# Kernel tuning notes

Measured on AMD Instinct MI355X. Metric: run time of the kernel, lower is better.

Reference implementation:

```python
import jax, jax.numpy as jnp
import numpy as np

B, T, DIN, H, HB = 256, 512, 64, 256, 128  # batch, seq, input, hidden, bi-hidden


def rnn_layer(x, wih, whh, bih, bhh):
    # PyTorch nn.RNN (tanh) layer, batch_first. x: [B,T,I] -> [B,T,H]
    xw = jnp.einsum('bti,hi->bth', x, wih) + bih
    h0 = jnp.zeros((x.shape[0], whh.shape[0]), x.dtype)
    def step(h, xt):
        h = jnp.tanh(xt + h @ whh.T + bhh)
        return h, h
    _, ys = jax.lax.scan(step, h0, jnp.swapaxes(xw, 0, 1))
    return jnp.swapaxes(ys, 0, 1)


def gru_layer(x, wih, whh, bih, bhh, reverse=False):
    # PyTorch nn.GRU layer (gate order r,z,n). x: [B,T,I] -> [B,T,Hh]
    Hh = whh.shape[1]
    xg = jnp.einsum('bti,gi->btg', x, wih) + bih  # [B,T,3Hh]
    h0 = jnp.zeros((x.shape[0], Hh), x.dtype)
    def step(h, xt):
        hg = h @ whh.T + bhh
        xr, xz, xn = jnp.split(xt, 3, axis=-1)
        hr, hz, hn = jnp.split(hg, 3, axis=-1)
        r = jax.nn.sigmoid(xr + hr)
        z = jax.nn.sigmoid(xz + hz)
        n = jnp.tanh(xn + r * hn)
        h = (1.0 - z) * n + z * h
        return h, h
    _, ys = jax.lax.scan(step, h0, jnp.swapaxes(xg, 0, 1), reverse=reverse)
    return jnp.swapaxes(ys, 0, 1)


def setup_inputs() -> dict:
    key = jax.random.key(0)
    ks = iter(jax.random.split(key, 40))
    s = 0.05
    def w(shape):
        return jax.random.normal(next(ks), shape, jnp.float32) * s
    inp = {"x": jax.random.normal(next(ks), (B, T, DIN), jnp.float32)}
    inp.update(dict(
        rnn_wih0=w((H, DIN)), rnn_whh0=w((H, H)), rnn_bih0=w((H,)), rnn_bhh0=w((H,)),
        rnn_wih1=w((H, H)), rnn_whh1=w((H, H)), rnn_bih1=w((H,)), rnn_bhh1=w((H,)),
        gru_wih=w((2, 3 * H, H)), gru_whh=w((2, 3 * H, H)),
        gru_bih=w((2, 3 * H)), gru_bhh=w((2, 3 * H)),
        # bi-GRU: index order [l0_fwd, l0_bwd, l1_fwd, l1_bwd]; all inputs have width H
        bi_wih=w((4, 3 * HB, H)), bi_whh=w((4, 3 * HB, HB)),
        bi_bih=w((4, 3 * HB)), bi_bhh=w((4, 3 * HB)),
        att_w1=w((H // 2, H)), att_b1=w((H // 2,)), att_w2=w((1, H // 2)), att_b2=w((1,)),
        bn_gamma=jnp.ones((H,), jnp.float32), bn_beta=jnp.zeros((H,), jnp.float32),
        bn_mean=jnp.zeros((H,), jnp.float32), bn_var=jnp.ones((H,), jnp.float32),
        fc_w1=w((H // 2, H)), fc_b1=w((H // 2,)),
        fc_w2=w((H // 4, H // 2)), fc_b2=w((H // 4,)),
        fc_w3=w((1, H // 4)), fc_b3=w((1,)),
    ))
    return inp


def reference(x, rnn_wih0, rnn_whh0, rnn_bih0, rnn_bhh0,
              rnn_wih1, rnn_whh1, rnn_bih1, rnn_bhh1,
              gru_wih, gru_whh, gru_bih, gru_bhh,
              bi_wih, bi_whh, bi_bih, bi_bhh,
              att_w1, att_b1, att_w2, att_b2,
              bn_gamma, bn_beta, bn_mean, bn_var,
              fc_w1, fc_b1, fc_w2, fc_b2, fc_w3, fc_b3):
    # --- stacked tanh RNN (2 layers); dropout is identity in eval ---
    h = rnn_layer(x, rnn_wih0, rnn_whh0, rnn_bih0, rnn_bhh0)
    h = rnn_layer(h, rnn_wih1, rnn_whh1, rnn_bih1, rnn_bhh1)
    # --- stacked GRU (2 layers) ---
    for l in range(2):
        h = gru_layer(h, gru_wih[l], gru_whh[l], gru_bih[l], gru_bhh[l])
    # --- bidirectional GRU (2 layers, hidden HB per direction) ---
    for l in range(2):
        f = gru_layer(h, bi_wih[2 * l], bi_whh[2 * l], bi_bih[2 * l], bi_bhh[2 * l])
        b = gru_layer(h, bi_wih[2 * l + 1], bi_whh[2 * l + 1], bi_bih[2 * l + 1], bi_bhh[2 * l + 1], reverse=True)
        h = jnp.concatenate([f, b], axis=-1)  # [B,T,H]
    # --- additive attention pooling over time ---
    scores = jnp.tanh(h @ att_w1.T + att_b1) @ att_w2.T + att_b2  # [B,T,1]
    weights = jax.nn.softmax(scores, axis=1)
    ctx = jnp.sum(weights * h, axis=1)  # [B,H]
    # --- batchnorm (eval mode: running stats) ---
    ctx = (ctx - bn_mean) / jnp.sqrt(bn_var + 1e-5) * bn_gamma + bn_beta
    # --- FC head ---
    o = jax.nn.relu(ctx @ fc_w1.T + fc_b1)
    o = jax.nn.relu(o @ fc_w2.T + fc_b2)
    return o @ fc_w3.T + fc_b3  # [B,1]
```

## Files before the change

### kernel.cpp

```cpp
#include <hip/hip_runtime.h>


typedef short sv8 __attribute__((ext_vector_type(8)));
typedef short sv4 __attribute__((ext_vector_type(4)));
typedef float fv4 __attribute__((ext_vector_type(4)));

__device__ __forceinline__ float bf2f(short s) {
  union { unsigned u; float f; } v; v.u = ((unsigned)(unsigned short)s) << 16; return v.f;
}
__device__ __forceinline__ short f2bf(float f) {
  union { float f; unsigned u; } v; v.f = f;
  unsigned r = (v.u + 0x7fffu + ((v.u >> 16) & 1u)) >> 16;
  return (short)r;
}
__device__ __forceinline__ float sigm(float x) { return 1.f / (1.f + __expf(-x)); }
__device__ __forceinline__ float tanh_f(float x) {
  float ax = fabsf(x);
  float e = __expf(2.f * ax);
  float t = 1.f - 2.f / (e + 1.f);
  return copysignf(t, x);
}

__global__ __launch_bounds__(256) void f2b4(const float* __restrict__ s,
                                            short* __restrict__ d, int n4) {
  int i = blockIdx.x * 256 + threadIdx.x;
  if (i < n4) {
    fv4 v = ((const fv4*)s)[i];
    sv4 o;
    o[0] = f2bf(v[0]); o[1] = f2bf(v[1]); o[2] = f2bf(v[2]); o[3] = f2bf(v[3]);
    ((sv4*)d)[i] = o;
  }
}

__global__ __launch_bounds__(256) void bias_prep(
    const float* __restrict__ rbih0, const float* __restrict__ rbhh0,
    const float* __restrict__ rbih1, const float* __restrict__ rbhh1,
    const float* __restrict__ gbih, const float* __restrict__ gbhh,
    const float* __restrict__ bbih, const float* __restrict__ bbhh,
    float* __restrict__ BC) {
  int i = blockIdx.x * 256 + threadIdx.x;
  if (i >= 3584) return;
  float v;
  if (i < 256)       v = rbih0[i] + rbhh0[i];
  else if (i < 512)  { int c = i - 256; v = rbih1[c] + rbhh1[c]; }
  else if (i < 2048) { int j = i - 512; int c = j % 768;
                       v = gbih[j] + (c < 512 ? gbhh[j] : 0.f); }
  else               { int j = i - 2048; int c = j % 384;
                       v = bbih[j] + (c < 256 ? bbhh[j] : 0.f); }
  BC[i] = v;
}

template <int KS, int ACT, bool AF32>
__global__ __launch_bounds__(256, 4) void gemm_xw(
    const void* __restrict__ Av, const short* __restrict__ W,
    const float* __restrict__ bias, short* __restrict__ C,
    int N, int ldc, int w0, int l2tc) {
  const int K = KS * 32;
  const int lane = threadIdx.x & 63, wv = threadIdx.x >> 6;
  const int l15 = lane & 15, q = lane >> 4;
  const int m0 = blockIdx.x * 128 + wv * 32;
  const int tcm = (1 << l2tc) - 1;

  sv8 af[2][KS];
#pragma unroll
  for (int s = 0; s < 2; ++s) {
    const int r = m0 + s * 16 + l15;
    const size_t arow = (size_t)(r >> l2tc) * 512 + w0 + (r & tcm);
    if (AF32) {
      const float* ap = (const float*)Av + arow * K + q * 8;
#pragma unroll
      for (int k = 0; k < KS; ++k) {
        fv4 lo = *(const fv4*)(ap + k * 32);
        fv4 hi = *(const fv4*)(ap + k * 32 + 4);
        sv8 o;
        o[0] = f2bf(lo[0]); o[1] = f2bf(lo[1]); o[2] = f2bf(lo[2]); o[3] = f2bf(lo[3]);
        o[4] = f2bf(hi[0]); o[5] = f2bf(hi[1]); o[6] = f2bf(hi[2]); o[7] = f2bf(hi[3]);
        af[s][k] = o;
      }
    } else {
      const short* ap = (const short*)Av + arow * K + q * 8;
#pragma unroll
      for (int k = 0; k < KS; ++k) af[s][k] = *(const sv8*)(ap + k * 32);
    }
  }
  const int N16 = N >> 4;
  for (int nt = 0; nt < N16; ++nt) {
    const short* wp = W + (size_t)(nt * 16 + l15) * K + q * 8;
    fv4 acc0 = {0.f, 0.f, 0.f, 0.f}, acc1 = {0.f, 0.f, 0.f, 0.f};
#pragma unroll
    for (int k = 0; k < KS; ++k) {
      sv8 bf = *(const sv8*)(wp + k * 32);
      acc0 = __builtin_amdgcn_mfma_f32_16x16x32_bf16(af[0][k], bf, acc0, 0, 0, 0);
      acc1 = __builtin_amdgcn_mfma_f32_16x16x32_bf16(af[1][k], bf, acc1, 0, 0, 0);
    }
    float bv = bias[nt * 16 + l15];
#pragma unroll
    for (int s = 0; s < 2; ++s) {
      fv4 a = s ? acc1 : acc0;
#pragma unroll
      for (int j = 0; j < 4; ++j) {
        float v = a[j] + bv;
        if (ACT == 1) v = tanh_f(v);
        int row = m0 + s * 16 + q * 4 + j;
        C[(size_t)row * ldc + nt * 16 + l15] = f2bf(v);
      }
    }
  }
}

__global__ __launch_bounds__(256, 1) void rnn_scan(
    const short* __restrict__ xg, const short* __restrict__ whh,
    short* __restrict__ hout, int w0, int Tc, int first,
    short* __restrict__ hst) {
  constexpr int T = 512, H = 256, NR = 8, SP = H + 8;
  __shared__ __align__(16) short hl[NR * H];
  __shared__ __align__(16) float S[NR * SP];
  const int tid = threadIdx.x, lane = tid & 63, wv = tid >> 6;
  const int l15 = lane & 15, q = lane >> 4;
  const int r0 = blockIdx.x * NR;

  sv8 wf[4][8];
#pragma unroll
  for (int s = 0; s < 4; ++s) {
    const short* wp = whh + (size_t)(wv * 64 + s * 16 + l15) * H + q * 8;
#pragma unroll
    for (int k = 0; k < 8; ++k) wf[s][k] = *(const sv8*)(wp + k * 32);
  }
  const int brow = tid >> 5, bcb = tid & 31;
  const int hlo = brow * H + ((bcb * 8) ^ (brow << 3));
  const size_t xbase = ((size_t)(r0 + brow) * Tc) * H + bcb * 8;
  const size_t obase = ((size_t)(r0 + brow) * T + w0) * H + bcb * 8;

  sv8 hvv;
  if (first) { sv8 z = {0,0,0,0,0,0,0,0}; hvv = z; }
  else hvv = *(const sv8*)(hst + (size_t)(r0 + brow) * H + bcb * 8);
  *(sv8*)&hl[hlo] = hvv;
  sv8 xr = *(const sv8*)(xg + xbase);
  __syncthreads();

  const int arow = l15 & 7;
  const short* hb = hl + arow * H;
  const int asw = arow << 3;

  for (int t = 0; t < Tc; ++t) {
    fv4 acc[4] = {{0,0,0,0},{0,0,0,0},{0,0,0,0},{0,0,0,0}};
#pragma unroll
    for (int k = 0; k < 8; ++k) {
      sv8 a = *(const sv8*)(hb + ((k * 32 + q * 8) ^ asw));
#pragma unroll
      for (int s = 0; s < 4; ++s)
        acc[s] = __builtin_amdgcn_mfma_f32_16x16x32_bf16(a, wf[s][k], acc[s], 0, 0, 0);
    }
    if (q < 2) {
#pragma unroll
      for (int s = 0; s < 4; ++s)
#pragma unroll
        for (int j = 0; j < 4; ++j)
          S[(q * 4 + j) * SP + wv * 64 + s * 16 + l15] = acc[s][j];
    }
    __syncthreads();
    const float* sp = &S[brow * SP + bcb * 8];
    fv4 slo = *(const fv4*)sp, shi = *(const fv4*)(sp + 4);
    sv8 o;
#pragma unroll
    for (int i = 0; i < 4; ++i) o[i] = f2bf(tanh_f(bf2f(xr[i]) + slo[i]));
#pragma unroll
    for (int i = 0; i < 4; ++i) o[4 + i] = f2bf(tanh_f(bf2f(xr[4 + i]) + shi[i]));
    hvv = o;
    *(sv8*)&hl[hlo] = o;
    *(sv8*)(hout + obase + (size_t)t * H) = o;
    if (t + 1 < Tc) xr = *(const sv8*)(xg + xbase + (size_t)(t + 1) * H);
    __syncthreads();
  }
  *(sv8*)(hst + (size_t)(r0 + brow) * H + bcb * 8) = hvv;
}

__global__ __launch_bounds__(256, 1) void gru_scan(
    const short* __restrict__ xg, const short* __restrict__ whh,
    const float* __restrict__ bhn, short* __restrict__ hout,
    int w0, int Tc, int first, short* __restrict__ hst) {
  constexpr int T = 512, H = 256, G = 768, NR = 8, SP = H + 8;
  __shared__ __align__(16) short hl[NR * H];
  __shared__ __align__(16) float S[3 * NR * SP];
  const int tid = threadIdx.x, lane = tid & 63, wv = tid >> 6;
  const int l15 = lane & 15, q = lane >> 4;
  const int r0 = blockIdx.x * NR;

  sv8 wf[3][4][8];
#pragma unroll
  for (int g = 0; g < 3; ++g)
#pragma unroll
    for (int s = 0; s < 4; ++s) {
      const short* wp = whh + (size_t)(g * H + wv * 64 + s * 16 + l15) * H + q * 8;
#pragma unroll
      for (int k = 0; k < 8; ++k) wf[g][s][k] = *(const sv8*)(wp + k * 32);
    }
  const int brow = tid >> 5, bcb = tid & 31;
  const int hlo = brow * H + ((bcb * 8) ^ (brow << 3));
  const size_t xbase = ((size_t)(r0 + brow) * Tc) * G + bcb * 8;
  const size_t obase = ((size_t)(r0 + brow) * T + w0) * H + bcb * 8;
  const float* bp = bhn + bcb * 8;
  fv4 bn0 = *(const fv4*)bp, bn1 = *(const fv4*)(bp + 4);

  sv8 hp;
  if (first) { sv8 z = {0,0,0,0,0,0,0,0}; hp = z; }
  else hp = *(const sv8*)(hst + (size_t)(r0 + brow) * H + bcb * 8);
  *(sv8*)&hl[hlo] = hp;
  sv8 xr0 = *(const sv8*)(xg + xbase);
  sv8 xr1 = *(const sv8*)(xg + xbase + 256);
  sv8 xr2 = *(const sv8*)(xg + xbase + 512);
  __syncthreads();

  const int arow = l15 & 7;
  const short* hb = hl + arow * H;
  const int asw = arow << 3;

  for (int t = 0; t < Tc; ++t) {
    fv4 acc[3][4];
#pragma unroll
    for (int g = 0; g < 3; ++g)
#pragma unroll
      for (int s = 0; s < 4; ++s) acc[g][s] = (fv4){0,0,0,0};
#pragma unroll
    for (int k = 0; k < 8; ++k) {
      sv8 a = *(const sv8*)(hb + ((k * 32 + q * 8) ^ asw));
#pragma unroll
      for (int g = 0; g < 3; ++g)
#pragma unroll
        for (int s = 0; s < 4; ++s)
          acc[g][s] = __builtin_amdgcn_mfma_f32_16x16x32_bf16(a, wf[g][s][k], acc[g][s], 0, 0, 0);
    }
    if (q < 2) {
#pragma unroll
      for (int g = 0; g < 3; ++g)
#pragma unroll
        for (int s = 0; s < 4; ++s)
#pragma unroll
          for (int j = 0; j < 4; ++j)
            S[(g * NR + q * 4 + j) * SP + wv * 64 + s * 16 + l15] = acc[g][s][j];
    }
    __syncthreads();
    const float* s0 = &S[(0 * NR + brow) * SP + bcb * 8];
    const float* s1 = &S[(1 * NR + brow) * SP + bcb * 8];
    const float* s2 = &S[(2 * NR + brow) * SP + bcb * 8];
    fv4 r0v = *(const fv4*)s0, r1v = *(const fv4*)(s0 + 4);
    fv4 z0v = *(const fv4*)s1, z1v = *(const fv4*)(s1 + 4);
    fv4 n0v = *(const fv4*)s2, n1v = *(const fv4*)(s2 + 4);
    sv8 o;
#pragma unroll
    for (int i = 0; i < 4; ++i) {
      float rr = sigm(bf2f(xr0[i]) + r0v[i]);
      float zz = sigm(bf2f(xr1[i]) + z0v[i]);
      float nn = tanh_f(bf2f(xr2[i]) + rr * (n0v[i] + bn0[i]));
      o[i] = f2bf((1.f - zz) * nn + zz * bf2f(hp[i]));
    }
#pragma unroll
    for (int i = 0; i < 4; ++i) {
      float rr = sigm(bf2f(xr0[4 + i]) + r1v[i]);
      float zz = sigm(bf2f(xr1[4 + i]) + z1v[i]);
      float nn = tanh_f(bf2f(xr2[4 + i]) + rr * (n1v[i] + bn1[i]));
      o[4 + i] = f2bf((1.f - zz) * nn + zz * bf2f(hp[4 + i]));
    }
    hp = o;
    *(sv8*)&hl[hlo] = o;
    *(sv8*)(hout + obase + (size_t)t * H) = o;
    if (t + 1 < Tc) {
      const size_t xb = xbase + (size_t)(t + 1) * G;
      xr0 = *(const sv8*)(xg + xb);
      xr1 = *(const sv8*)(xg + xb + 256);
      xr2 = *(const sv8*)(xg + xb + 512);
    }
    __syncthreads();
  }
  *(sv8*)(hst + (size_t)(r0 + brow) * H + bcb * 8) = hp;
}

__global__ __launch_bounds__(256, 1) void bigru_scan(
    const short* __restrict__ xgf, const short* __restrict__ xgb,
    const short* __restrict__ whh_f, const short* __restrict__ whh_b,
    const float* __restrict__ bhn_f, const float* __restrict__ bhn_b,
    short* __restrict__ hout, int w0f, int w0b, int Tc, int first,
    short* __restrict__ hstf, short* __restrict__ hstb) {
  constexpr int T = 512, HB = 128, GL = 384, NR = 8, SP = HB + 8, HO = 256;
  __shared__ __align__(16) short hl[NR * HB];
  __shared__ __align__(16) float S[3 * NR * SP];
  const int tid = threadIdx.x, lane = tid & 63, wv = tid >> 6;
  const int l15 = lane & 15, q = lane >> 4;
  const int dir = blockIdx.x >> 5;
  const int r0 = (blockIdx.x & 31) * NR;
  const short* whh = dir ? whh_b : whh_f;
  const short* xg  = dir ? xgb : xgf;
  const float* bhn = dir ? bhn_b : bhn_f;
  short* hst = dir ? hstb : hstf;
  const int w0 = dir ? w0b : w0f;

  sv8 wf[3][2][4];
#pragma unroll
  for (int g = 0; g < 3; ++g)
#pragma unroll
    for (int s = 0; s < 2; ++s) {
      const short* wp = whh + (size_t)(g * HB + wv * 32 + s * 16 + l15) * HB + q * 8;
#pragma unroll
      for (int k = 0; k < 4; ++k) wf[g][s][k] = *(const sv8*)(wp + k * 32);
    }
  const int brow = tid >> 5, bcb = tid & 31;
  const int hlo = brow * HB + ((bcb * 4) ^ (brow << 3));
  const size_t xbase = ((size_t)(r0 + brow) * Tc) * GL + bcb * 4;
  const size_t obase = ((size_t)(r0 + brow) * T + w0) * HO + dir * HB + bcb * 4;
  fv4 bn = *(const fv4*)(bhn + bcb * 4);

  sv4 hp;
  if (first) { sv4 z = {0,0,0,0}; hp = z; }
  else hp = *(const sv4*)(hst + (size_t)(r0 + brow) * HB + bcb * 4);
  *(sv4*)&hl[hlo] = hp;
  int tl = dir ? (Tc - 1) : 0;
  sv4 xr0 = *(const sv4*)(xg + xbase + (size_t)tl * GL);
  sv4 xr1 = *(const sv4*)(xg + xbase + (size_t)tl * GL + 128);
  sv4 xr2 = *(const sv4*)(xg + xbase + (size_t)tl * GL + 256);
  __syncthreads();

  const int arow = l15 & 7;
  const short* hb = hl + arow * HB;
  const int asw = arow << 3;

  for (int t = 0; t < Tc; ++t) {
    tl = dir ? (Tc - 1 - t) : t;
    fv4 acc[3][2];
#pragma unroll
    for (int g = 0; g < 3; ++g)
#pragma unroll
      for (int s = 0; s < 2; ++s) acc[g][s] = (fv4){0,0,0,0};
#pragma unroll
    for (int k = 0; k < 4; ++k) {
      sv8 a = *(const sv8*)(hb + ((k * 32 + q * 8) ^ asw));
#pragma unroll
      for (int g = 0; g < 3; ++g)
#pragma unroll
        for (int s = 0; s < 2; ++s)
          acc[g][s] = __builtin_amdgcn_mfma_f32_16x16x32_bf16(a, wf[g][s][k], acc[g][s], 0, 0, 0);
    }
    if (q < 2) {
#pragma unroll
      for (int g = 0; g < 3; ++g)
#pragma unroll
        for (int s = 0; s < 2; ++s)
#pragma unroll
          for (int j = 0; j < 4; ++j)
            S[(g * NR + q * 4 + j) * SP + wv * 32 + s * 16 + l15] = acc[g][s][j];
    }
    __syncthreads();
    fv4 sr = *(const fv4*)&S[(0 * NR + brow) * SP + bcb * 4];
    fv4 sz = *(const fv4*)&S[(1 * NR + brow) * SP + bcb * 4];
    fv4 sn = *(const fv4*)&S[(2 * NR + brow) * SP + bcb * 4];
    sv4 o;
#pragma unroll
    for (int i = 0; i < 4; ++i) {
      float rr = sigm(bf2f(xr0[i]) + sr[i]);
      float zz = sigm(bf2f(xr1[i]) + sz[i]);
      float nn = tanh_f(bf2f(xr2[i]) + rr * (sn[i] + bn[i]));
      o[i] = f2bf((1.f - zz) * nn + zz * bf2f(hp[i]));
    }
    hp = o;
    *(sv4*)&hl[hlo] = o;
    *(sv4*)(hout + obase + (size_t)tl * HO) = o;
    if (t + 1 < Tc) {
      const int tn = dir ? (Tc - 2 - t) : (t + 1);
      const size_t xb = xbase + (size_t)tn * GL;
      xr0 = *(const sv4*)(xg + xb);
      xr1 = *(const sv4*)(xg + xb + 128);
      xr2 = *(const sv4*)(xg + xb + 256);
    }
    __syncthreads();
  }
  *(sv4*)(hst + (size_t)(r0 + brow) * HB + bcb * 4) = hp;
}

__global__ __launch_bounds__(256) void att_scores(
    const short* __restrict__ s1, const float* __restrict__ w2,
    const float* __restrict__ b2, float* __restrict__ sc, int w0, int l2tc) {
  const int r = blockIdx.x * 256 + threadIdx.x;
  const int b = r >> l2tc, tl = r & ((1 << l2tc) - 1);
  const short* p = s1 + (size_t)r * 128;
  float sum = 0.f;
#pragma unroll
  for (int c = 0; c < 16; ++c) {
    sv8 v = *(const sv8*)(p + c * 8);
#pragma unroll
    for (int j = 0; j < 8; ++j) sum += bf2f(v[j]) * w2[c * 8 + j];
  }
  sc[b * 512 + w0 + tl] = sum + b2[0];
}

__global__ __launch_bounds__(256) void pool_head(
    const float* __restrict__ sc, const short* __restrict__ h,
    const float* __restrict__ bng, const float* __restrict__ bnb,
    const float* __restrict__ bnm, const float* __restrict__ bnv,
    const float* __restrict__ w1, const float* __restrict__ b1,
    const float* __restrict__ w2, const float* __restrict__ b2,
    const float* __restrict__ w3, const float* __restrict__ b3,
    float* __restrict__ out) {
  constexpr int T = 512, H = 256;
  __shared__ float wts[T];
  __shared__ float red[4];
  __shared__ float ctxs[H];
  __shared__ float o1[128];
  __shared__ float o2[64];
  const int b = blockIdx.x, tid = threadIdx.x, lane = tid & 63, wv = tid >> 6;

  float s0 = sc[b * T + tid], s1v = sc[b * T + 256 + tid];
  float m = fmaxf(s0, s1v);
#pragma unroll
  for (int o = 32; o >= 1; o >>= 1) m = fmaxf(m, __shfl_xor(m, o));
  if (lane == 0) red[wv] = m;
  __syncthreads();
  m = fmaxf(fmaxf(red[0], red[1]), fmaxf(red[2], red[3]));

  float e0 = __expf(s0 - m), e1 = __expf(s1v - m);
  wts[tid] = e0; wts[tid + 256] = e1;
  float se = e0 + e1;
#pragma unroll
  for (int o = 32; o >= 1; o >>= 1) se += __shfl_xor(se, o);
  __syncthreads();
  if (lane == 0) red[wv] = se;
  __syncthreads();
  const float Z = red[0] + red[1] + red[2] + red[3];

  float cx = 0.f;
  const short* hp = h + (size_t)b * T * H + tid;
  for (int t = 0; t < T; ++t) cx += wts[t] * bf2f(hp[(size_t)t * H]);
  cx /= Z;
  cx = (cx - bnm[tid]) * rsqrtf(bnv[tid] + 1e-5f) * bng[tid] + bnb[tid];
  ctxs[tid] = cx;
  __syncthreads();

  if (tid < 128) {
    const float* wr = w1 + tid * H;
    float a = 0.f;
#pragma unroll 8
    for (int k = 0; k < H; ++k) a += ctxs[k] * wr[k];
    o1[tid] = fmaxf(a + b1[tid], 0.f);
  }
  __syncthreads();
  if (tid < 64) {
    const float* wr = w2 + tid * 128;
    float a = 0.f;
#pragma unroll 8
    for (int k = 0; k < 128; ++k) a += o1[k] * wr[k];
    o2[tid] = fmaxf(a + b2[tid], 0.f);
  }
  __syncthreads();
  if (tid < 64) {
    float p = o2[tid] * w3[tid];
#pragma unroll
    for (int o = 32; o >= 1; o >>= 1) p += __shfl_xor(p, o);
    if (tid == 0) out[b] = p + b3[0];
  }
}

extern "C" void kernel_launch(void* const* d_in, const int* in_sizes, int n_in,
                              void* d_out, int out_size, void* d_ws, size_t ws_size,
                              hipStream_t stream) {
  const float* x_f    = (const float*)d_in[0];
  const float* rwih0  = (const float*)d_in[1];
  const float* rwhh0  = (const float*)d_in[2];
  const float* rbih0  = (const float*)d_in[3];
  const float* rbhh0  = (const float*)d_in[4];
  const float* rwih1  = (const float*)d_in[5];
  const float* rwhh1  = (const float*)d_in[6];
  const float* rbih1  = (const float*)d_in[7];
  const float* rbhh1  = (const float*)d_in[8];
  const float* gwih_f = (const float*)d_in[9];
  const float* gwhh_f = (const float*)d_in[10];
  const float* gbih   = (const float*)d_in[11];
  const float* gbhh   = (const float*)d_in[12];
  const float* bwih_f = (const float*)d_in[13];
  const float* bwhh_f = (const float*)d_in[14];
  const float* bbih   = (const float*)d_in[15];
  const float* bbhh   = (const float*)d_in[16];
  const float* aw1_f  = (const float*)d_in[17];
  const float* ab1    = (const float*)d_in[18];
  const float* aw2    = (const float*)d_in[19];
  const float* ab2    = (const float*)d_in[20];
  const float* bng    = (const float*)d_in[21];
  const float* bnb    = (const float*)d_in[22];
  const float* bnm    = (const float*)d_in[23];
  const float* bnv    = (const float*)d_in[24];
  const float* fw1    = (const float*)d_in[25];
  const float* fb1    = (const float*)d_in[26];
  const float* fw2    = (const float*)d_in[27];
  const float* fb2    = (const float*)d_in[28];
  const float* fw3    = (const float*)d_in[29];
  const float* fb3    = (const float*)d_in[30];
  (void)in_sizes; (void)n_in; (void)out_size;

  char* ws = (char*)d_ws;
  size_t off = 0;
  auto take = [&](size_t bytes) -> char* {
    char* p = ws + off;
    off += (bytes + 255) & ~(size_t)255;
    return p;
  };
  short* wih0 = (short*)take(16384 * 2);
  short* whh0 = (short*)take(65536 * 2);
  short* wih1 = (short*)take(65536 * 2);
  short* whh1 = (short*)take(65536 * 2);
  short* gwih = (short*)take(393216 * 2);
  short* gwhh = (short*)take(393216 * 2);
  short* bwih = (short*)take(393216 * 2);
  short* bwhh = (short*)take(196608 * 2);
  short* aw1  = (short*)take(32768 * 2);
  float* BC   = (float*)take(3584 * 4);
  short* hstA = (short*)take(65536 * 2);
  short* hstF = (short*)take(32768 * 2);
  short* hstB = (short*)take(32768 * 2);
  float* SC   = (float*)take(131072ull * 4);
  short* H1   = (short*)take(131072ull * 256 * 2);
  short* H2   = (short*)take(131072ull * 256 * 2);

  const size_t region = ws_size > off ? ws_size - off : 0;
  const size_t XGF = 131072ull * 768 * 2;
  int NC;
  if      (region >= XGF)      NC = 1;
  else if (region >= XGF / 2)  NC = 2;
  else if (region >= XGF / 4)  NC = 4;
  else if (region >= XGF / 8)  NC = 8;
  else if (region >= XGF / 16) NC = 16;
  else                         NC = 32;
  const int Tc = 512 / NC;
  int l2 = 0; while ((1 << l2) < Tc) ++l2;
  short* XG  = (short*)(ws + off);
  short* XGb = XG + (size_t)256 * Tc * 384;

#define CONV(src, dst, n) f2b4<<<(n) / 1024, 256, 0, stream>>>(src, dst, (n) / 4)
  CONV(rwih0, wih0, 16384);
  CONV(rwhh0, whh0, 65536);
  CONV(rwih1, wih1, 65536);
  CONV(rwhh1, whh1, 65536);
  CONV(gwih_f, gwih, 393216);
  CONV(gwhh_f, gwhh, 393216);
  CONV(bwih_f, bwih, 393216);
  CONV(bwhh_f, bwhh, 196608);
  CONV(aw1_f, aw1, 32768);
#undef CONV
  bias_prep<<<14, 256, 0, stream>>>(rbih0, rbhh0, rbih1, rbhh1,
                                    gbih, gbhh, bbih, bbhh, BC);

  const int gg = 2 * Tc;

  for (int c = 0; c < NC; ++c) {
    gemm_xw<2, 0, true><<<gg, 256, 0, stream>>>(x_f, wih0, BC, XG, 256, 256, c * Tc, l2);
    rnn_scan<<<32, 256, 0, stream>>>(XG, whh0, H1, c * Tc, Tc, c == 0, hstA);
  }
  for (int c = 0; c < NC; ++c) {
    gemm_xw<8, 0, false><<<gg, 256, 0, stream>>>(H1, wih1, BC + 256, XG, 256, 256, c * Tc, l2);
    rnn_scan<<<32, 256, 0, stream>>>(XG, whh1, H1, c * Tc, Tc, c == 0, hstA);
  }
  for (int c = 0; c < NC; ++c) {
    gemm_xw<8, 0, false><<<gg, 256, 0, stream>>>(H1, gwih, BC + 512, XG, 768, 768, c * Tc, l2);
    gru_scan<<<32, 256, 0, stream>>>(XG, gwhh, gbhh + 512, H1, c * Tc, Tc, c == 0, hstA);
  }
  for (int c = 0; c < NC; ++c) {
    gemm_xw<8, 0, false><<<gg, 256, 0, stream>>>(H1, gwih + 196608, BC + 1280, XG, 768, 768, c * Tc, l2);
    gru_scan<<<32, 256, 0, stream>>>(XG, gwhh + 196608, gbhh + 768 + 512, H1, c * Tc, Tc, c == 0, hstA);
  }
  for (int s = 0; s < NC; ++s) {
    const int w0f = s * Tc, w0b = (NC - 1 - s) * Tc;
    gemm_xw<8, 0, false><<<gg, 256, 0, stream>>>(H1, bwih, BC + 2048, XG, 384, 384, w0f, l2);
    gemm_xw<8, 0, false><<<gg, 256, 0, stream>>>(H1, bwih + 98304, BC + 2432, XGb, 384, 384, w0b, l2);
    bigru_scan<<<64, 256, 0, stream>>>(XG, XGb, bwhh, bwhh + 49152,
                                       bbhh + 256, bbhh + 384 + 256,
                                       H2, w0f, w0b, Tc, s == 0, hstF, hstB);
  }
  for (int s = 0; s < NC; ++s) {
    const int w0f = s * Tc, w0b = (NC - 1 - s) * Tc;
    gemm_xw<8, 0, false><<<gg, 256, 0, stream>>>(H2, bwih + 2 * 98304, BC + 2816, XG, 384, 384, w0f, l2);
    gemm_xw<8, 0, false><<<gg, 256, 0, stream>>>(H2, bwih + 3 * 98304, BC + 3200, XGb, 384, 384, w0b, l2);
    bigru_scan<<<64, 256, 0, stream>>>(XG, XGb, bwhh + 2 * 49152, bwhh + 3 * 49152,
                                       bbhh + 2 * 384 + 256, bbhh + 3 * 384 + 256,
                                       H1, w0f, w0b, Tc, s == 0, hstF, hstB);
  }
  for (int c = 0; c < NC; ++c) {
    gemm_xw<8, 1, false><<<gg, 256, 0, stream>>>(H1, aw1, ab1, XG, 128, 128, c * Tc, l2);
    att_scores<<<Tc, 256, 0, stream>>>(XG, aw2, ab2, SC, c * Tc, l2);
  }
  pool_head<<<256, 256, 0, stream>>>(SC, H1, bng, bnb, bnm, bnv,
                                     fw1, fb1, fw2, fb2, fw3, fb3, (float*)d_out);
}
```

Measured before the change: 5.614 ms.

## Double scan kernel block size to 8 waves, splitting recurrent weight columns wider

The RNN, GRU and bi-GRU scan kernels now launch 512 threads (8 waves) per block instead of 256. Each wave holds half as many recurrent-weight MFMA fragments and computes fewer output columns per step, and the elementwise gate update is re-mapped so each wave handles one batch row. The gate shared-memory buffer becomes a single fused [NR x 3H] array. The aim is to shorten the per-timestep serial MFMA chain and cut register pressure on the latency-bound recurrence, at the cost of more waves joining each per-step barrier and narrower vector loads and stores.

New measurement: 5.503 ms. -2.0%, faster.

```diff
diff --git a/kernel.cpp b/kernel.cpp
--- a/kernel.cpp
+++ b/kernel.cpp
@@ -3,7 +3,9 @@
 
 typedef short sv8 __attribute__((ext_vector_type(8)));
 typedef short sv4 __attribute__((ext_vector_type(4)));
+typedef short sv2 __attribute__((ext_vector_type(2)));
 typedef float fv4 __attribute__((ext_vector_type(4)));
+typedef float fv2 __attribute__((ext_vector_type(2)));
 
 __device__ __forceinline__ float bf2f(short s) {
   union { unsigned u; float f; } v; v.u = ((unsigned)(unsigned short)s) << 16; return v.f;
@@ -108,7 +110,7 @@
   }
 }
 
-__global__ __launch_bounds__(256, 1) void rnn_scan(
+__global__ __launch_bounds__(512, 2) void rnn_scan(
     const short* __restrict__ xg, const short* __restrict__ whh,
     short* __restrict__ hout, int w0, int Tc, int first,
     short* __restrict__ hst) {
@@ -119,23 +121,24 @@
   const int l15 = lane & 15, q = lane >> 4;
   const int r0 = blockIdx.x * NR;
 
-  sv8 wf[4][8];
-#pragma unroll
-  for (int s = 0; s < 4; ++s) {
-    const short* wp = whh + (size_t)(wv * 64 + s * 16 + l15) * H + q * 8;
+  sv8 wf[2][8];
+#pragma unroll
+  for (int s = 0; s < 2; ++s) {
+    const short* wp = whh + (size_t)(wv * 32 + s * 16 + l15) * H + q * 8;
 #pragma unroll
     for (int k = 0; k < 8; ++k) wf[s][k] = *(const sv8*)(wp + k * 32);
   }
-  const int brow = tid >> 5, bcb = tid & 31;
-  const int hlo = brow * H + ((bcb * 8) ^ (brow << 3));
-  const size_t xbase = ((size_t)(r0 + brow) * Tc) * H + bcb * 8;
-  const size_t obase = ((size_t)(r0 + brow) * T + w0) * H + bcb * 8;
-
-  sv8 hvv;
-  if (first) { sv8 z = {0,0,0,0,0,0,0,0}; hvv = z; }
-  else hvv = *(const sv8*)(hst + (size_t)(r0 + brow) * H + bcb * 8);
-  *(sv8*)&hl[hlo] = hvv;
-  sv8 xr = *(const sv8*)(xg + xbase);
+  const int row = wv;
+  const int c = (tid & 63) * 4;
+  const size_t xbase = ((size_t)(r0 + row) * Tc) * H + c;
+  const size_t obase = ((size_t)(r0 + row) * T + w0) * H + c;
+  const int hlo = row * H + (c ^ (row << 3));
+
+  sv4 hp;
+  if (first) { sv4 z = {0,0,0,0}; hp = z; }
+  else hp = *(const sv4*)(hst + (size_t)(r0 + row) * H + c);
+  *(sv4*)&hl[hlo] = hp;
+  sv4 xr = *(const sv4*)(xg + xbase);
   __syncthreads();
 
   const int arow = l15 & 7;
@@ -143,72 +146,67 @@
   const int asw = arow << 3;
 
   for (int t = 0; t < Tc; ++t) {
-    fv4 acc[4] = {{0,0,0,0},{0,0,0,0},{0,0,0,0},{0,0,0,0}};
+    fv4 acc[2] = {{0,0,0,0},{0,0,0,0}};
 #pragma unroll
     for (int k = 0; k < 8; ++k) {
       sv8 a = *(const sv8*)(hb + ((k * 32 + q * 8) ^ asw));
 #pragma unroll
-      for (int s = 0; s < 4; ++s)
+      for (int s = 0; s < 2; ++s)
         acc[s] = __builtin_amdgcn_mfma_f32_16x16x32_bf16(a, wf[s][k], acc[s], 0, 0, 0);
     }
     if (q < 2) {
 #pragma unroll
-      for (int s = 0; s < 4; ++s)
+      for (int s = 0; s < 2; ++s)
 #pragma unroll
         for (int j = 0; j < 4; ++j)
-          S[(q * 4 + j) * SP + wv * 64 + s * 16 + l15] = acc[s][j];
+          S[(q * 4 + j) * SP + wv * 32 + s * 16 + l15] = acc[s][j];
     }
     __syncthreads();
-    const float* sp = &S[brow * SP + bcb * 8];
-    fv4 slo = *(const fv4*)sp, shi = *(const fv4*)(sp + 4);
-    sv8 o;
-#pragma unroll
-    for (int i = 0; i < 4; ++i) o[i] = f2bf(tanh_f(bf2f(xr[i]) + slo[i]));
-#pragma unroll
-    for (int i = 0; i < 4; ++i) o[4 + i] = f2bf(tanh_f(bf2f(xr[4 + i]) + shi[i]));
-    hvv = o;
-    *(sv8*)&hl[hlo] = o;
-    *(sv8*)(hout + obase + (size_t)t * H) = o;
-    if (t + 1 < Tc) xr = *(const sv8*)(xg + xbase + (size_t)(t + 1) * H);
+    fv4 sv = *(const fv4*)&S[row * SP + c];
+    sv4 o;
+#pragma unroll
+    for (int i = 0; i < 4; ++i) o[i] = f2bf(tanh_f(bf2f(xr[i]) + sv[i]));
+    hp = o;
+    *(sv4*)&hl[hlo] = o;
+    *(sv4*)(hout + obase + (size_t)t * H) = o;
+    if (t + 1 < Tc) xr = *(const sv4*)(xg + xbase + (size_t)(t + 1) * H);
     __syncthreads();
   }
-  *(sv8*)(hst + (size_t)(r0 + brow) * H + bcb * 8) = hvv;
-}
-
-__global__ __launch_bounds__(256, 1) void gru_scan(
+  *(sv4*)(hst + (size_t)(r0 + row) * H + c) = hp;
+}
+
+__global__ __launch_bounds__(512, 2) void gru_scan(
     const short* __restrict__ xg, const short* __restrict__ whh,
     const float* __restrict__ bhn, short* __restrict__ hout,
     int w0, int Tc, int first, short* __restrict__ hst) {
-  constexpr int T = 512, H = 256, G = 768, NR = 8, SP = H + 8;
+  constexpr int T = 512, H = 256, G = 768, NR = 8, SP = G + 8;
   __shared__ __align__(16) short hl[NR * H];
-  __shared__ __align__(16) float S[3 * NR * SP];
+  __shared__ __align__(16) float S[NR * SP];
   const int tid = threadIdx.x, lane = tid & 63, wv = tid >> 6;
   const int l15 = lane & 15, q = lane >> 4;
   const int r0 = blockIdx.x * NR;
 
-  sv8 wf[3][4][8];
-#pragma unroll
-  for (int g = 0; g < 3; ++g)
-#pragma unroll
-    for (int s = 0; s < 4; ++s) {
-      const short* wp = whh + (size_t)(g * H + wv * 64 + s * 16 + l15) * H + q * 8;
-#pragma unroll
-      for (int k = 0; k < 8; ++k) wf[g][s][k] = *(const sv8*)(wp + k * 32);
-    }
-  const int brow = tid >> 5, bcb = tid & 31;
-  const int hlo = brow * H + ((bcb * 8) ^ (brow << 3));
-  const size_t xbase = ((size_t)(r0 + brow) * Tc) * G + bcb * 8;
-  const size_t obase = ((size_t)(r0 + brow) * T + w0) * H + bcb * 8;
-  const float* bp = bhn + bcb * 8;
-  fv4 bn0 = *(const fv4*)bp, bn1 = *(const fv4*)(bp + 4);
-
-  sv8 hp;
-  if (first) { sv8 z = {0,0,0,0,0,0,0,0}; hp = z; }
-  else hp = *(const sv8*)(hst + (size_t)(r0 + brow) * H + bcb * 8);
-  *(sv8*)&hl[hlo] = hp;
-  sv8 xr0 = *(const sv8*)(xg + xbase);
-  sv8 xr1 = *(const sv8*)(xg + xbase + 256);
-  sv8 xr2 = *(const sv8*)(xg + xbase + 512);
+  sv8 wf[6][8];
+#pragma unroll
+  for (int s = 0; s < 6; ++s) {
+    const short* wp = whh + (size_t)(wv * 96 + s * 16 + l15) * H + q * 8;
+#pragma unroll
+    for (int k = 0; k < 8; ++k) wf[s][k] = *(const sv8*)(wp + k * 32);
+  }
+  const int row = wv;
+  const int c = (tid & 63) * 4;
+  const size_t xbase = ((size_t)(r0 + row) * Tc) * G + c;
+  const size_t obase = ((size_t)(r0 + row) * T + w0) * H + c;
+  const int hlo = row * H + (c ^ (row << 3));
+  fv4 bn = *(const fv4*)(bhn + c);
+
+  sv4 hp;
+  if (first) { sv4 z = {0,0,0,0}; hp = z; }
+  else hp = *(const sv4*)(hst + (size_t)(r0 + row) * H + c);
+  *(sv4*)&hl[hlo] = hp;
+  sv4 xr0 = *(const sv4*)(xg + xbase);
+  sv4 xr1 = *(const sv4*)(xg + xbase + 256);
+  sv4 xr2 = *(const sv4*)(xg + xbase + 512);
   __syncthreads();
 
   const int arow = l15 & 7;
@@ -216,74 +214,58 @@
   const int asw = arow << 3;
 
   for (int t = 0; t < Tc; ++t) {
-    fv4 acc[3][4];
-#pragma unroll
-    for (int g = 0; g < 3; ++g)
-#pragma unroll
-      for (int s = 0; s < 4; ++s) acc[g][s] = (fv4){0,0,0,0};
+    fv4 acc[6];
+#pragma unroll
+    for (int s = 0; s < 6; ++s) acc[s] = (fv4){0,0,0,0};
 #pragma unroll
     for (int k = 0; k < 8; ++k) {
       sv8 a = *(const sv8*)(hb + ((k * 32 + q * 8) ^ asw));
 #pragma unroll
-      for (int g = 0; g < 3; ++g)
-#pragma unroll
-        for (int s = 0; s < 4; ++s)
-          acc[g][s] = __builtin_amdgcn_mfma_f32_16x16x32_bf16(a, wf[g][s][k], acc[g][s], 0, 0, 0);
+      for (int s = 0; s < 6; ++s)
+        acc[s] = __builtin_amdgcn_mfma_f32_16x16x32_bf16(a, wf[s][k], acc[s], 0, 0, 0);
     }
     if (q < 2) {
 #pragma unroll
-      for (int g = 0; g < 3; ++g)
-#pragma unroll
-        for (int s = 0; s < 4; ++s)
-#pragma unroll
-          for (int j = 0; j < 4; ++j)
-            S[(g * NR + q * 4 + j) * SP + wv * 64 + s * 16 + l15] = acc[g][s][j];
+      for (int s = 0; s < 6; ++s)
+#pragma unroll
+        for (int j = 0; j < 4; ++j)
+          S[(q * 4 + j) * SP + wv * 96 + s * 16 + l15] = acc[s][j];
     }
     __syncthreads();
-    const float* s0 = &S[(0 * NR + brow) * SP + bcb * 8];
-    const float* s1 = &S[(1 * NR + brow) * SP + bcb * 8];
-    const float* s2 = &S[(2 * NR + brow) * SP + bcb * 8];
-    fv4 r0v = *(const fv4*)s0, r1v = *(const fv4*)(s0 + 4);
-    fv4 z0v = *(const fv4*)s1, z1v = *(const fv4*)(s1 + 4);
-    fv4 n0v = *(const fv4*)s2, n1v = *(const fv4*)(s2 + 4);
-    sv8 o;
+    fv4 sr = *(const fv4*)&S[row * SP + c];
+    fv4 sz = *(const fv4*)&S[row * SP + c + 256];
+    fv4 sn = *(const fv4*)&S[row * SP + c + 512];
+    sv4 o;
 #pragma unroll
     for (int i = 0; i < 4; ++i) {
-      float rr = sigm(bf2f(xr0[i]) + r0v[i]);
-      float zz = sigm(bf2f(xr1[i]) + z0v[i]);
-      float nn = tanh_f(bf2f(xr2[i]) + rr * (n0v[i] + bn0[i]));
+      float rr = sigm(bf2f(xr0[i]) + sr[i]);
+      float zz = sigm(bf2f(xr1[i]) + sz[i]);
+      float nn = tanh_f(bf2f(xr2[i]) + rr * (sn[i] + bn[i]));
       o[i] = f2bf((1.f - zz) * nn + zz * bf2f(hp[i]));
     }
-#pragma unroll
-    for (int i = 0; i < 4; ++i) {
-      float rr = sigm(bf2f(xr0[4 + i]) + r1v[i]);
-      float zz = sigm(bf2f(xr1[4 + i]) + z1v[i]);
-      float nn = tanh_f(bf2f(xr2[4 + i]) + rr * (n1v[i] + bn1[i]));
-      o[4 + i] = f2bf((1.f - zz) * nn + zz * bf2f(hp[4 + i]));
-    }
     hp = o;
-    *(sv8*)&hl[hlo] = o;
-    *(sv8*)(hout + obase + (size_t)t * H) = o;
+    *(sv4*)&hl[hlo] = o;
+    *(sv4*)(hout + obase + (size_t)t * H) = o;
     if (t + 1 < Tc) {
       const size_t xb = xbase + (size_t)(t + 1) * G;
-      xr0 = *(const sv8*)(xg + xb);
-      xr1 = *(const sv8*)(xg + xb + 256);
-      xr2 = *(const sv8*)(xg + xb + 512);
+      xr0 = *(const sv4*)(xg + xb);
+      xr1 = *(const sv4*)(xg + xb + 256);
+      xr2 = *(const sv4*)(xg + xb + 512);
     }
     __syncthreads();
   }
-  *(sv8*)(hst + (size_t)(r0 + brow) * H + bcb * 8) = hp;
-}
-
-__global__ __launch_bounds__(256, 1) void bigru_scan(
+  *(sv4*)(hst + (size_t)(r0 + row) * H + c) = hp;
+}
+
+__global__ __launch_bounds__(512, 2) void bigru_scan(
     const short* __restrict__ xgf, const short* __restrict__ xgb,
     const short* __restrict__ whh_f, const short* __restrict__ whh_b,
     const float* __restrict__ bhn_f, const float* __restrict__ bhn_b,
     short* __restrict__ hout, int w0f, int w0b, int Tc, int first,
     short* __restrict__ hstf, short* __restrict__ hstb) {
-  constexpr int T = 512, HB = 128, GL = 384, NR = 8, SP = HB + 8, HO = 256;
+  constexpr int T = 512, HB = 128, GL = 384, NR = 8, SP = GL + 8, HO = 256;
   __shared__ __align__(16) short hl[NR * HB];
-  __shared__ __align__(16) float S[3 * NR * SP];
+  __shared__ __align__(16) float S[NR * SP];
   const int tid = threadIdx.x, lane = tid & 63, wv = tid >> 6;
   const int l15 = lane & 15, q = lane >> 4;
   const int dir = blockIdx.x >> 5;
@@ -294,29 +276,28 @@
   short* hst = dir ? hstb : hstf;
   const int w0 = dir ? w0b : w0f;
 
-  sv8 wf[3][2][4];
-#pragma unroll
-  for (int g = 0; g < 3; ++g)
-#pragma unroll
-    for (int s = 0; s < 2; ++s) {
-      const short* wp = whh + (size_t)(g * HB + wv * 32 + s * 16 + l15) * HB + q * 8;
-#pragma unroll
-      for (int k = 0; k < 4; ++k) wf[g][s][k] = *(const sv8*)(wp + k * 32);
-    }
-  const int brow = tid >> 5, bcb = tid & 31;
-  const int hlo = brow * HB + ((bcb * 4) ^ (brow << 3));
-  const size_t xbase = ((size_t)(r0 + brow) * Tc) * GL + bcb * 4;
-  const size_t obase = ((size_t)(r0 + brow) * T + w0) * HO + dir * HB + bcb * 4;
-  fv4 bn = *(const fv4*)(bhn + bcb * 4);
-
-  sv4 hp;
-  if (first) { sv4 z = {0,0,0,0}; hp = z; }
-  else hp = *(const sv4*)(hst + (size_t)(r0 + brow) * HB + bcb * 4);
-  *(sv4*)&hl[hlo] = hp;
+  sv8 wf[3][4];
+#pragma unroll
+  for (int s = 0; s < 3; ++s) {
+    const short* wp = whh + (size_t)(wv * 48 + s * 16 + l15) * HB + q * 8;
+#pragma unroll
+    for (int k = 0; k < 4; ++k) wf[s][k] = *(const sv8*)(wp + k * 32);
+  }
+  const int row = wv;
+  const int c = (tid & 63) * 2;
+  const size_t xbase = ((size_t)(r0 + row) * Tc) * GL + c;
+  const size_t obase = ((size_t)(r0 + row) * T + w0) * HO + dir * HB + c;
+  const int hlo = row * HB + (c ^ (row << 3));
+  fv2 bn = *(const fv2*)(bhn + c);
+
+  sv2 hp;
+  if (first) { sv2 z = {0,0}; hp = z; }
+  else hp = *(const sv2*)(hst + (size_t)(r0 + row) * HB + c);
+  *(sv2*)&hl[hlo] = hp;
   int tl = dir ? (Tc - 1) : 0;
-  sv4 xr0 = *(const sv4*)(xg + xbase + (size_t)tl * GL);
-  sv4 xr1 = *(const sv4*)(xg + xbase + (size_t)tl * GL + 128);
-  sv4 xr2 = *(const sv4*)(xg + xbase + (size_t)tl * GL + 256);
+  sv2 xr0 = *(const sv2*)(xg + xbase + (size_t)tl * GL);
+  sv2 xr1 = *(const sv2*)(xg + xbase + (size_t)tl * GL + 128);
+  sv2 xr2 = *(const sv2*)(xg + xbase + (size_t)tl * GL + 256);
   __syncthreads();
 
   const int arow = l15 & 7;
@@ -325,54 +306,48 @@
 
   for (int t = 0; t < Tc; ++t) {
     tl = dir ? (Tc - 1 - t) : t;
-    fv4 acc[3][2];
-#pragma unroll
-    for (int g = 0; g < 3; ++g)
-#pragma unroll
-      for (int s = 0; s < 2; ++s) acc[g][s] = (fv4){0,0,0,0};
+    fv4 acc[3];
+#pragma unroll
+    for (int s = 0; s < 3; ++s) acc[s] = (fv4){0,0,0,0};
 #pragma unroll
     for (int k = 0; k < 4; ++k) {
       sv8 a = *(const sv8*)(hb + ((k * 32 + q * 8) ^ asw));
 #pragma unroll
-      for (int g = 0; g < 3; ++g)
-#pragma unroll
-        for (int s = 0; s < 2; ++s)
-          acc[g][s] = __builtin_amdgcn_mfma_f32_16x16x32_bf16(a, wf[g][s][k], acc[g][s], 0, 0, 0);
+      for (int s = 0; s < 3; ++s)
+        acc[s] = __builtin_amdgcn_mfma_f32_16x16x32_bf16(a, wf[s][k], acc[s], 0, 0, 0);
     }
     if (q < 2) {
 #pragma unroll
-      for (int g = 0; g < 3; ++g)
-#pragma unroll
-        for (int s = 0; s < 2; ++s)
-#pragma unroll
-          for (int j = 0; j < 4; ++j)
-            S[(g * NR + q * 4 + j) * SP + wv * 32 + s * 16 + l15] = acc[g][s][j];
+      for (int s = 0; s < 3; ++s)
+#pragma unroll
+        for (int j = 0; j < 4; ++j)
+          S[(q * 4 + j) * SP + wv * 48 + s * 16 + l15] = acc[s][j];
     }
     __syncthreads();
-    fv4 sr = *(const fv4*)&S[(0 * NR + brow) * SP + bcb * 4];
-    fv4 sz = *(const fv4*)&S[(1 * NR + brow) * SP + bcb * 4];
-    fv4 sn = *(const fv4*)&S[(2 * NR + brow) * SP + bcb * 4];
-    sv4 o;
-#pragma unroll
-    for (int i = 0; i < 4; ++i) {
+    fv2 sr = *(const fv2*)&S[row * SP + c];
+    fv2 sz = *(const fv2*)&S[row * SP + c + 128];
+    fv2 sn = *(const fv2*)&S[row * SP + c + 256];
+    sv2 o;
+#pragma unroll
+    for (int i = 0; i < 2; ++i) {
       float rr = sigm(bf2f(xr0[i]) + sr[i]);
       float zz = sigm(bf2f(xr1[i]) + sz[i]);
       float nn = tanh_f(bf2f(xr2[i]) + rr * (sn[i] + bn[i]));
       o[i] = f2bf((1.f - zz) * nn + zz * bf2f(hp[i]));
     }
     hp = o;
-    *(sv4*)&hl[hlo] = o;
-    *(sv4*)(hout + obase + (size_t)tl * HO) = o;
+    *(sv2*)&hl[hlo] = o;
+    *(sv2*)(hout + obase + (size_t)tl * HO) = o;
     if (t + 1 < Tc) {
       const int tn = dir ? (Tc - 2 - t) : (t + 1);
       const size_t xb = xbase + (size_t)tn * GL;
-      xr0 = *(const sv4*)(xg + xb);
-      xr1 = *(const sv4*)(xg + xb + 128);
-      xr2 = *(const sv4*)(xg + xb + 256);
+      xr0 = *(const sv2*)(xg + xb);
+      xr1 = *(const sv2*)(xg + xb + 128);
+      xr2 = *(const sv2*)(xg + xb + 256);
     }
     __syncthreads();
   }
-  *(sv4*)(hst + (size_t)(r0 + brow) * HB + bcb * 4) = hp;
+  *(sv2*)(hst + (size_t)(r0 + row) * HB + c) = hp;
 }
 
 __global__ __launch_bounds__(256) void att_scores(
@@ -549,25 +524,25 @@
 
   for (int c = 0; c < NC; ++c) {
     gemm_xw<2, 0, true><<<gg, 256, 0, stream>>>(x_f, wih0, BC, XG, 256, 256, c * Tc, l2);
-    rnn_scan<<<32, 256, 0, stream>>>(XG, whh0, H1, c * Tc, Tc, c == 0, hstA);
+    rnn_scan<<<32, 512, 0, stream>>>(XG, whh0, H1, c * Tc, Tc, c == 0, hstA);
   }
   for (int c = 0; c < NC; ++c) {
     gemm_xw<8, 0, false><<<gg, 256, 0, stream>>>(H1, wih1, BC + 256, XG, 256, 256, c * Tc, l2);
-    rnn_scan<<<32, 256, 0, stream>>>(XG, whh1, H1, c * Tc, Tc, c == 0, hstA);
+    rnn_scan<<<32, 512, 0, stream>>>(XG, whh1, H1, c * Tc, Tc, c == 0, hstA);
   }
   for (int c = 0; c < NC; ++c) {
     gemm_xw<8, 0, false><<<gg, 256, 0, stream>>>(H1, gwih, BC + 512, XG, 768, 768, c * Tc, l2);
-    gru_scan<<<32, 256, 0, stream>>>(XG, gwhh, gbhh + 512, H1, c * Tc, Tc, c == 0, hstA);
+    gru_scan<<<32, 512, 0, stream>>>(XG, gwhh, gbhh + 512, H1, c * Tc, Tc, c == 0, hstA);
   }
   for (int c = 0; c < NC; ++c) {
     gemm_xw<8, 0, false><<<gg, 256, 0, stream>>>(H1, gwih + 196608, BC + 1280, XG, 768, 768, c * Tc, l2);
-    gru_scan<<<32, 256, 0, stream>>>(XG, gwhh + 196608, gbhh + 768 + 512, H1, c * Tc, Tc, c == 0, hstA);
+    gru_scan<<<32, 512, 0, stream>>>(XG, gwhh + 196608, gbhh + 768 + 512, H1, c * Tc, Tc, c == 0, hstA);
   }
   for (int s = 0; s < NC; ++s) {
     const int w0f = s * Tc, w0b = (NC - 1 - s) * Tc;
     gemm_xw<8, 0, false><<<gg, 256, 0, stream>>>(H1, bwih, BC + 2048, XG, 384, 384, w0f, l2);
     gemm_xw<8, 0, false><<<gg, 256, 0, stream>>>(H1, bwih + 98304, BC + 2432, XGb, 384, 384, w0b, l2);
-    bigru_scan<<<64, 256, 0, stream>>>(XG, XGb, bwhh, bwhh + 49152,
+    bigru_scan<<<64, 512, 0, stream>>>(XG, XGb, bwhh, bwhh + 49152,
                                        bbhh + 256, bbhh + 384 + 256,
                                        H2, w0f, w0b, Tc, s == 0, hstF, hstB);
   }
@@ -575,7 +550,7 @@
     const int w0f = s * Tc, w0b = (NC - 1 - s) * Tc;
     gemm_xw<8, 0, false><<<gg, 256, 0, stream>>>(H2, bwih + 2 * 98304, BC + 2816, XG, 384, 384, w0f, l2);
     gemm_xw<8, 0, false><<<gg, 256, 0, stream>>>(H2, bwih + 3 * 98304, BC + 3200, XGb, 384, 384, w0b, l2);
-    bigru_scan<<<64, 256, 0, stream>>>(XG, XGb, bwhh + 2 * 49152, bwhh + 3 * 49152,
+    bigru_scan<<<64, 512, 0, stream>>>(XG, XGb, bwhh + 2 * 49152, bwhh + 3 * 49152,
                                        bbhh + 2 * 384 + 256, bbhh + 3 * 384 + 256,
                                        H1, w0f, w0b, Tc, s == 0, hstF, hstB);
   }
```
